# Kernel optimization log

Hardware: AMD Instinct MI355X
Metric: run time of the kernel (lower is better)

Reference implementation:

```python
import jax, jax.numpy as jnp
import numpy as np

D_MODEL = 1024
N_HEADS = 16
HEAD_DIM = D_MODEL // N_HEADS


def setup_inputs() -> dict:
    key = jax.random.key(0)
    ks = jax.random.split(key, 5)
    s = 1.0 / np.sqrt(D_MODEL)
    return {
        "x": jax.random.normal(ks[0], (2, 2048, D_MODEL), dtype=jnp.float32),
        "w_qkv": jax.random.uniform(ks[1], (3 * D_MODEL, D_MODEL), jnp.float32, -s, s),
        "b_qkv": jax.random.uniform(ks[2], (3 * D_MODEL,), jnp.float32, -s, s),
        "w_out": jax.random.uniform(ks[3], (D_MODEL, D_MODEL), jnp.float32, -s, s),
        "b_out": jax.random.uniform(ks[4], (D_MODEL,), jnp.float32, -s, s),
    }


def _attn(x, w_qkv, b_qkv, w_out, b_out):
    bsz, seq_len, _ = x.shape
    qkv = jnp.einsum('bsd,ed->bse', x, w_qkv) + b_qkv  # [B,S,3D]
    q, k, v = jnp.split(qkv, 3, axis=-1)
    def heads(t):  # [B,S,D] -> [B,H,S,Dh]
        return t.reshape(bsz, seq_len, N_HEADS, HEAD_DIM).transpose(0, 2, 1, 3)
    q, k, v = heads(q), heads(k), heads(v)
    scores = jnp.einsum('bhqd,bhkd->bhqk', q, k) / np.sqrt(HEAD_DIM)
    mask = jnp.tril(jnp.ones((seq_len, seq_len), dtype=bool))
    scores = jnp.where(mask, scores, -jnp.inf)
    probs = jax.nn.softmax(scores, axis=-1)
    attn = jnp.einsum('bhqk,bhkd->bhqd', probs, v)
    attn = attn.transpose(0, 2, 1, 3).reshape(bsz, seq_len, D_MODEL)
    return jnp.einsum('bsd,ed->bse', attn, w_out) + b_out


def reference(x, w_qkv, b_qkv, w_out, b_out):
    return _attn(x, w_qkv, b_qkv, w_out, b_out)
```

## Files before the change

kernel.cpp:

```cpp
#include <hip/hip_runtime.h>
#include <hip/hip_bf16.h>
#include <stdint.h>

#define SEQ     2048
#define BATCH   2
#define NHEADS  16
#define HDIM    64
#define DMODEL  1024
#define N3      3072
#define D2      2048
#define MTOT    (BATCH*SEQ)

typedef __attribute__((ext_vector_type(4))) float f32x4;
typedef __attribute__((ext_vector_type(8))) short bf16x8;

static __device__ inline unsigned short f2bf(float f) {
    union { float f; unsigned u; } v; v.f = f;
    unsigned r = (v.u + 0x7fffu + ((v.u >> 16) & 1u)) >> 16;
    return (unsigned short)r;
}
static __device__ inline unsigned pk2bf(float a, float b) {
    union { __hip_bfloat162 h; unsigned u; } c;
    c.h = __float22bfloat162_rn(make_float2(a, b));
    return c.u;
}

#define GLDS(gp, lp) __builtin_amdgcn_global_load_lds( \
    (const __attribute__((address_space(1))) void*)(gp), \
    (__attribute__((address_space(3))) void*)(lp), 16, 0, 0)

__global__ void cast_all(const float* __restrict__ x,
                         const float* __restrict__ wqkv,
                         const float* __restrict__ wout,
                         unsigned short* __restrict__ xb,
                         unsigned short* __restrict__ wqkvb,
                         unsigned short* __restrict__ woutb) {
    long i4 = (long)(blockIdx.x * blockDim.x + threadIdx.x) * 4;
    const float* src; unsigned short* dst; long off;
    if (i4 < 4194304L)      { src = x;    dst = xb;    off = i4; }
    else if (i4 < 7340032L) { src = wqkv; dst = wqkvb; off = i4 - 4194304L; }
    else                    { src = wout; dst = woutb; off = i4 - 7340032L; }
    float4 v = *(const float4*)(src + off);
    union { uint2 u; ushort4 s; } pk;
    pk.u.x = pk2bf(v.x, v.y); pk.u.y = pk2bf(v.z, v.w);
    *(ushort4*)(dst + off) = pk.s;
}

__global__ __launch_bounds__(256, 2) void gemm_qkv(
    const unsigned short* __restrict__ A,
    const unsigned short* __restrict__ B,
    const float* __restrict__ bias,
    unsigned short* __restrict__ qk,
    unsigned short* __restrict__ vT)
{
    __shared__ __align__(16) unsigned short sA[2][128][64];
    __shared__ __align__(16) unsigned short sB[2][128][64];
    const int tid  = threadIdx.x;
    const int wave = tid >> 6, lane = tid & 63;
    const int quad = lane >> 4, l16 = lane & 15, l7 = l16 & 7;
    const int wm = wave >> 1, wn = wave & 1;
    const int m0 = blockIdx.x * 128, n0 = blockIdx.y * 128;

    f32x4 acc[4][4];
    const f32x4 zero = {0.f, 0.f, 0.f, 0.f};
    #pragma unroll
    for (int i = 0; i < 4; i++)
        #pragma unroll
        for (int j = 0; j < 4; j++) acc[i][j] = zero;

    const int rsel = tid >> 3;
    const int sgl  = (tid & 7) ^ (rsel & 7);
    const unsigned short* gA0 = A + (long)(m0 + rsel) * 1024 + sgl * 8;
    const unsigned short* gB0 = B + (long)(n0 + rsel) * 1024 + sgl * 8;

    #pragma unroll
    for (int i = 0; i < 4; i++) {
        GLDS(gA0 + (long)(32 * i) * 1024, &sA[0][32 * i + wave * 8][0]);
        GLDS(gB0 + (long)(32 * i) * 1024, &sB[0][32 * i + wave * 8][0]);
    }

    int buf = 0;
    for (int k0 = 0; k0 < 1024; k0 += 64, buf ^= 1) {
        __syncthreads();
        if (k0 + 64 < 1024) {
            #pragma unroll
            for (int i = 0; i < 4; i++) {
                GLDS(gA0 + (long)(32 * i) * 1024 + k0 + 64, &sA[buf ^ 1][32 * i + wave * 8][0]);
                GLDS(gB0 + (long)(32 * i) * 1024 + k0 + 64, &sB[buf ^ 1][32 * i + wave * 8][0]);
            }
        }
        #pragma unroll
        for (int ks = 0; ks < 2; ks++) {
            bf16x8 af[4], bfr[4];
            #pragma unroll
            for (int mt = 0; mt < 4; mt++)
                af[mt] = *(const bf16x8*)(&sA[buf][wm * 64 + mt * 16 + l16][((ks * 4 + quad) ^ l7) * 8]);
            #pragma unroll
            for (int nt = 0; nt < 4; nt++)
                bfr[nt] = *(const bf16x8*)(&sB[buf][wn * 64 + nt * 16 + l16][((ks * 4 + quad) ^ l7) * 8]);
            #pragma unroll
            for (int mt = 0; mt < 4; mt++)
                #pragma unroll
                for (int nt = 0; nt < 4; nt++)
                    acc[mt][nt] = __builtin_amdgcn_mfma_f32_16x16x32_bf16(
                        af[mt], bfr[nt], acc[mt][nt], 0, 0, 0);
        }
    }

    if (n0 < 2048) {
        #pragma unroll
        for (int nt = 0; nt < 4; nt++) {
            const int n_g = n0 + wn * 64 + nt * 16 + l16;
            const float bv = bias[n_g];
            #pragma unroll
            for (int mt = 0; mt < 4; mt++) {
                #pragma unroll
                for (int r = 0; r < 4; r++) {
                    const int m_g = m0 + wm * 64 + mt * 16 + quad * 4 + r;
                    qk[(long)m_g * D2 + n_g] = f2bf(acc[mt][nt][r] + bv);
                }
            }
        }
    } else {
        const int b = m0 >> 11;
        #pragma unroll
        for (int nt = 0; nt < 4; nt++) {
            const int n_g = n0 + wn * 64 + nt * 16 + l16;
            const int dm = n_g - 2048;
            const long vrow = (long)(((b << 4) + (dm >> 6)) << 6) + (dm & 63);
            const float bv = bias[n_g];
            #pragma unroll
            for (int mt = 0; mt < 4; mt++) {
                const int m_g = m0 + wm * 64 + mt * 16 + quad * 4;
                union { uint2 u; ushort4 s; } pk;
                pk.u.x = pk2bf(acc[mt][nt][0] + bv, acc[mt][nt][1] + bv);
                pk.u.y = pk2bf(acc[mt][nt][2] + bv, acc[mt][nt][3] + bv);
                *(ushort4*)(vT + vrow * D2 + (m_g & 2047)) = pk.s;
            }
        }
    }
}

__global__ __launch_bounds__(256, 2) void gemm_out(
    const unsigned short* __restrict__ A,
    const unsigned short* __restrict__ B,
    const float* __restrict__ bias,
    float* __restrict__ C)
{
    __shared__ __align__(16) unsigned short sA[2][128][64];
    __shared__ __align__(16) unsigned short sB[2][64][64];
    const int tid  = threadIdx.x;
    const int wave = tid >> 6, lane = tid & 63;
    const int quad = lane >> 4, l16 = lane & 15, l7 = l16 & 7;
    const int wm = wave >> 1, wn = wave & 1;
    const int m0 = blockIdx.x * 128, n0 = blockIdx.y * 64;

    f32x4 acc[4][2];
    const f32x4 zero = {0.f, 0.f, 0.f, 0.f};
    #pragma unroll
    for (int i = 0; i < 4; i++) { acc[i][0] = zero; acc[i][1] = zero; }

    const int rsel = tid >> 3;
    const int sgl  = (tid & 7) ^ (rsel & 7);
    const unsigned short* gA0 = A + (long)(m0 + rsel) * 1024 + sgl * 8;
    const unsigned short* gB0 = B + (long)(n0 + rsel) * 1024 + sgl * 8;

    #pragma unroll
    for (int i = 0; i < 4; i++)
        GLDS(gA0 + (long)(32 * i) * 1024, &sA[0][32 * i + wave * 8][0]);
    #pragma unroll
    for (int i = 0; i < 2; i++)
        GLDS(gB0 + (long)(32 * i) * 1024, &sB[0][32 * i + wave * 8][0]);

    int buf = 0;
    for (int k0 = 0; k0 < 1024; k0 += 64, buf ^= 1) {
        __syncthreads();
        if (k0 + 64 < 1024) {
            #pragma unroll
            for (int i = 0; i < 4; i++)
                GLDS(gA0 + (long)(32 * i) * 1024 + k0 + 64, &sA[buf ^ 1][32 * i + wave * 8][0]);
            #pragma unroll
            for (int i = 0; i < 2; i++)
                GLDS(gB0 + (long)(32 * i) * 1024 + k0 + 64, &sB[buf ^ 1][32 * i + wave * 8][0]);
        }
        #pragma unroll
        for (int ks = 0; ks < 2; ks++) {
            bf16x8 af[4], bfr[2];
            #pragma unroll
            for (int mt = 0; mt < 4; mt++)
                af[mt] = *(const bf16x8*)(&sA[buf][wm * 64 + mt * 16 + l16][((ks * 4 + quad) ^ l7) * 8]);
            #pragma unroll
            for (int nt = 0; nt < 2; nt++)
                bfr[nt] = *(const bf16x8*)(&sB[buf][wn * 32 + nt * 16 + l16][((ks * 4 + quad) ^ l7) * 8]);
            #pragma unroll
            for (int mt = 0; mt < 4; mt++)
                #pragma unroll
                for (int nt = 0; nt < 2; nt++)
                    acc[mt][nt] = __builtin_amdgcn_mfma_f32_16x16x32_bf16(
                        af[mt], bfr[nt], acc[mt][nt], 0, 0, 0);
        }
    }
    #pragma unroll
    for (int nt = 0; nt < 2; nt++) {
        const int n_g = n0 + wn * 32 + nt * 16 + l16;
        const float bv = bias[n_g];
        #pragma unroll
        for (int mt = 0; mt < 4; mt++) {
            #pragma unroll
            for (int r = 0; r < 4; r++) {
                const int m_g = m0 + wm * 64 + mt * 16 + quad * 4 + r;
                C[(long)m_g * DMODEL + n_g] = acc[mt][nt][r] + bv;
            }
        }
    }
}

__global__ __launch_bounds__(256, 2) void attn_kernel(
    const unsigned short* __restrict__ qk,
    const unsigned short* __restrict__ vT,
    unsigned short* __restrict__ attn)
{
    __shared__ __align__(16) unsigned short sK [2][2][64][64];
    __shared__ __align__(16) unsigned short sVt[2][2][64][64];
    __shared__ __align__(16) unsigned short sP [4][16][64];

    const int tid  = threadIdx.x;
    const int w    = tid >> 6, lane = tid & 63;
    const int quad = lane >> 4, l16 = lane & 15, l7 = l16 & 7;

    const int bh = blockIdx.x;
    const int b  = bh >> 4, h = bh & 15;
    const int pair = blockIdx.y;
    const long rowb = (long)b * SEQ;

    const int rl = lane >> 3;
    const int sm = (lane & 7) ^ rl;
    const unsigned short* kg = qk + (rowb + w * 16 + rl) * D2 + 1024 + h * HDIM + sm * 8;
    const unsigned short* vg = vT + (long)(bh * 64 + w * 16 + rl) * D2 + sm * 8;

    const int s0 = quad ^ l7;
    const float C2 = 0.18033688011112042f;
    const f32x4 zero = {0.f, 0.f, 0.f, 0.f};

    #pragma unroll
    for (int ph = 0; ph < 2; ph++) {
        const int qtile  = ph ? (31 - pair) : pair;
        const int qbase  = qtile * 64;
        const int ntiles = qtile + 1;
        const int npairs = (ntiles + 1) >> 1;

        bf16x8 qf0, qf1;
        {
            const unsigned short* qp = qk + (rowb + qbase + w * 16 + l16) * D2 + h * HDIM;
            qf0 = *(const bf16x8*)(qp + quad * 8);
            qf1 = *(const bf16x8*)(qp + 32 + quad * 8);
        }
        f32x4 Oacc[4];
        #pragma unroll
        for (int mf = 0; mf < 4; mf++) Oacc[mf] = zero;
        float l_i = 0.f;

        __syncthreads();
        {
            const long o0 = 0, o1 = (long)(1 <= qtile ? 1 : qtile) * 64;
            GLDS(kg + o0 * D2,           &sK [0][0][w * 16][0]);
            GLDS(kg + o0 * D2 + 8L * D2, &sK [0][0][w * 16 + 8][0]);
            GLDS(vg + o0,                &sVt[0][0][w * 16][0]);
            GLDS(vg + o0 + 8L * D2,      &sVt[0][0][w * 16 + 8][0]);
            GLDS(kg + o1 * D2,           &sK [0][1][w * 16][0]);
            GLDS(kg + o1 * D2 + 8L * D2, &sK [0][1][w * 16 + 8][0]);
            GLDS(vg + o1,                &sVt[0][1][w * 16][0]);
            GLDS(vg + o1 + 8L * D2,      &sVt[0][1][w * 16 + 8][0]);
        }

        int buf = 0;
        for (int p = 0; p < npairs; p++, buf ^= 1) {
            __syncthreads();
            if (p + 1 < npairs) {
                const int t0 = 2 * p + 2, t1 = 2 * p + 3;
                const long o0 = (long)(t0 <= qtile ? t0 : qtile) * 64;
                const long o1 = (long)(t1 <= qtile ? t1 : qtile) * 64;
                GLDS(kg + o0 * D2,           &sK [buf ^ 1][0][w * 16][0]);
                GLDS(kg + o0 * D2 + 8L * D2, &sK [buf ^ 1][0][w * 16 + 8][0]);
                GLDS(vg + o0,                &sVt[buf ^ 1][0][w * 16][0]);
                GLDS(vg + o0 + 8L * D2,      &sVt[buf ^ 1][0][w * 16 + 8][0]);
                GLDS(kg + o1 * D2,           &sK [buf ^ 1][1][w * 16][0]);
                GLDS(kg + o1 * D2 + 8L * D2, &sK [buf ^ 1][1][w * 16 + 8][0]);
                GLDS(vg + o1,                &sVt[buf ^ 1][1][w * 16][0]);
                GLDS(vg + o1 + 8L * D2,      &sVt[buf ^ 1][1][w * 16 + 8][0]);
            }
            #pragma unroll
            for (int s = 0; s < 2; s++) {
                const int t = 2 * p + s;
                if (t >= ntiles) break;

                f32x4 st[4];
                #pragma unroll
                for (int kvf = 0; kvf < 4; kvf++) {
                    bf16x8 kf0 = *(const bf16x8*)(&sK[buf][s][kvf * 16 + l16][s0 * 8]);
                    bf16x8 kf1 = *(const bf16x8*)(&sK[buf][s][kvf * 16 + l16][(s0 ^ 4) * 8]);
                    st[kvf] = __builtin_amdgcn_mfma_f32_16x16x32_bf16(kf0, qf0, zero, 0, 0, 0);
                    st[kvf] = __builtin_amdgcn_mfma_f32_16x16x32_bf16(kf1, qf1, st[kvf], 0, 0, 0);
                }
                if (t == qtile) {
                    const int ql = w * 16 + l16;
                    #pragma unroll
                    for (int kvf = 0; kvf < 4; kvf++) {
                        const int kv = kvf * 16 + quad * 4;
                        #pragma unroll
                        for (int r = 0; r < 4; r++)
                            if (kv + r > ql) st[kvf][r] = -1e30f;
                    }
                }
                #pragma unroll
                for (int kvf = 0; kvf < 4; kvf++) {
                    #pragma unroll
                    for (int r = 0; r < 4; r++)
                        st[kvf][r] = __builtin_amdgcn_exp2f(st[kvf][r] * C2);
                }
                f32x4 ps = (st[0] + st[1]) + (st[2] + st[3]);
                l_i += (ps[0] + ps[1]) + (ps[2] + ps[3]);

                #pragma unroll
                for (int kvf = 0; kvf < 4; kvf++) {
                    union { uint2 u; ushort4 s4; } pk;
                    pk.u.x = pk2bf(st[kvf][0], st[kvf][1]);
                    pk.u.y = pk2bf(st[kvf][2], st[kvf][3]);
                    const int seg = (kvf * 2 + (quad >> 1)) ^ l7;
                    *(ushort4*)(&sP[w][l16][seg * 8 + (quad & 1) * 4]) = pk.s4;
                }
                bf16x8 pf0 = *(const bf16x8*)(&sP[w][l16][(quad ^ l7) * 8]);
                bf16x8 pf1 = *(const bf16x8*)(&sP[w][l16][((4 + quad) ^ l7) * 8]);
                #pragma unroll
                for (int mf = 0; mf < 4; mf++) {
                    bf16x8 vf0 = *(const bf16x8*)(&sVt[buf][s][mf * 16 + l16][s0 * 8]);
                    bf16x8 vf1 = *(const bf16x8*)(&sVt[buf][s][mf * 16 + l16][(s0 ^ 4) * 8]);
                    Oacc[mf] = __builtin_amdgcn_mfma_f32_16x16x32_bf16(vf0, pf0, Oacc[mf], 0, 0, 0);
                    Oacc[mf] = __builtin_amdgcn_mfma_f32_16x16x32_bf16(vf1, pf1, Oacc[mf], 0, 0, 0);
                }
            }
        }
        float L = l_i;
        L += __shfl_xor(L, 16);
        L += __shfl_xor(L, 32);
        const float inv = 1.0f / L;
        const int q = qbase + w * 16 + l16;
        unsigned short* op = attn + (rowb + q) * DMODEL + h * HDIM + quad * 4;
        #pragma unroll
        for (int mf = 0; mf < 4; mf++) {
            union { uint2 u; ushort4 s4; } pk;
            pk.u.x = pk2bf(Oacc[mf][0] * inv, Oacc[mf][1] * inv);
            pk.u.y = pk2bf(Oacc[mf][2] * inv, Oacc[mf][3] * inv);
            *(ushort4*)(op + mf * 16) = pk.s4;
        }
    }
}

extern "C" void kernel_launch(void* const* d_in, const int* in_sizes, int n_in,
                              void* d_out, int out_size, void* d_ws, size_t ws_size,
                              hipStream_t stream) {
    const float* x    = (const float*)d_in[0];
    const float* wqkv = (const float*)d_in[1];
    const float* bqkv = (const float*)d_in[2];
    const float* wout = (const float*)d_in[3];
    const float* bout = (const float*)d_in[4];

    char* ws = (char*)d_ws;
    unsigned short* xb    = (unsigned short*)(ws);
    unsigned short* wqkvb = (unsigned short*)(ws + (8L << 20));
    unsigned short* woutb = (unsigned short*)(ws + (14L << 20));
    unsigned short* qkb   = (unsigned short*)(ws + (16L << 20));
    unsigned short* vTb   = (unsigned short*)(ws + (32L << 20));
    unsigned short* attnb = (unsigned short*)(ws + (40L << 20));

    cast_all<<<8192, 256, 0, stream>>>(x, wqkv, wout, xb, wqkvb, woutb);

    dim3 g1(32, 24);
    gemm_qkv<<<g1, 256, 0, stream>>>(xb, wqkvb, bqkv, qkb, vTb);

    dim3 g2(32, 16);
    attn_kernel<<<g2, 256, 0, stream>>>(qkb, vTb, attnb);

    dim3 g3(32, 16);
    gemm_out<<<g3, 256, 0, stream>>>(attnb, woutb, bout, (float*)d_out);
}
```

Before: 175.6 us.

## Enlarge QKV GEMM tiles to 256x256 with 8 waves and explicit waitcnt pipelining

The QKV projection GEMM now uses 256x256 output tiles per 512-thread block, with each wave owning a 128x64 sub-tile. Blocks are numbered M-fastest over a 1D grid. The main loop issues the next K-tile's global-to-LDS loads before computing the current one, using manual vmcnt/lgkmcnt waits and raw s_barriers instead of __syncthreads. The aim is more operand reuse per LDS load and fewer, larger blocks (192 instead of 768), at the cost of one block per CU and higher register pressure from 32 accumulators per lane.

```diff
diff --git a/kernel.cpp b/kernel.cpp
--- a/kernel.cpp
+++ b/kernel.cpp
@@ -46,66 +46,98 @@
     *(ushort4*)(dst + off) = pk.s;
 }
 
-__global__ __launch_bounds__(256, 2) void gemm_qkv(
+__global__ __launch_bounds__(512, 1) void gemm_qkv(
     const unsigned short* __restrict__ A,
     const unsigned short* __restrict__ B,
     const float* __restrict__ bias,
     unsigned short* __restrict__ qk,
     unsigned short* __restrict__ vT)
 {
-    __shared__ __align__(16) unsigned short sA[2][128][64];
-    __shared__ __align__(16) unsigned short sB[2][128][64];
+    __shared__ __align__(16) unsigned short sA[2][256][64];
+    __shared__ __align__(16) unsigned short sB[2][256][64];
     const int tid  = threadIdx.x;
-    const int wave = tid >> 6, lane = tid & 63;
+    const int w    = tid >> 6, lane = tid & 63;
     const int quad = lane >> 4, l16 = lane & 15, l7 = l16 & 7;
-    const int wm = wave >> 1, wn = wave & 1;
-    const int m0 = blockIdx.x * 128, n0 = blockIdx.y * 128;
-
-    f32x4 acc[4][4];
+    const int wm = w >> 2, wn = w & 3;
+    const int bid = blockIdx.x;
+    const int m0 = (bid & 15) << 8;
+    const int n0 = (bid >> 4) << 8;
+
+    f32x4 acc[8][4];
     const f32x4 zero = {0.f, 0.f, 0.f, 0.f};
     #pragma unroll
-    for (int i = 0; i < 4; i++)
+    for (int i = 0; i < 8; i++)
         #pragma unroll
         for (int j = 0; j < 4; j++) acc[i][j] = zero;
 
     const int rsel = tid >> 3;
     const int sgl  = (tid & 7) ^ (rsel & 7);
-    const unsigned short* gA0 = A + (long)(m0 + rsel) * 1024 + sgl * 8;
-    const unsigned short* gB0 = B + (long)(n0 + rsel) * 1024 + sgl * 8;
-
-    #pragma unroll
-    for (int i = 0; i < 4; i++) {
-        GLDS(gA0 + (long)(32 * i) * 1024, &sA[0][32 * i + wave * 8][0]);
-        GLDS(gB0 + (long)(32 * i) * 1024, &sB[0][32 * i + wave * 8][0]);
-    }
-
-    int buf = 0;
-    for (int k0 = 0; k0 < 1024; k0 += 64, buf ^= 1) {
-        __syncthreads();
-        if (k0 + 64 < 1024) {
-            #pragma unroll
-            for (int i = 0; i < 4; i++) {
-                GLDS(gA0 + (long)(32 * i) * 1024 + k0 + 64, &sA[buf ^ 1][32 * i + wave * 8][0]);
-                GLDS(gB0 + (long)(32 * i) * 1024 + k0 + 64, &sB[buf ^ 1][32 * i + wave * 8][0]);
-            }
-        }
-        #pragma unroll
-        for (int ks = 0; ks < 2; ks++) {
-            bf16x8 af[4], bfr[4];
-            #pragma unroll
-            for (int mt = 0; mt < 4; mt++)
-                af[mt] = *(const bf16x8*)(&sA[buf][wm * 64 + mt * 16 + l16][((ks * 4 + quad) ^ l7) * 8]);
-            #pragma unroll
-            for (int nt = 0; nt < 4; nt++)
-                bfr[nt] = *(const bf16x8*)(&sB[buf][wn * 64 + nt * 16 + l16][((ks * 4 + quad) ^ l7) * 8]);
-            #pragma unroll
-            for (int mt = 0; mt < 4; mt++)
-                #pragma unroll
-                for (int nt = 0; nt < 4; nt++)
-                    acc[mt][nt] = __builtin_amdgcn_mfma_f32_16x16x32_bf16(
-                        af[mt], bfr[nt], acc[mt][nt], 0, 0, 0);
-        }
-    }
+    const unsigned short* gA = A + (long)(m0 + rsel) * 1024 + sgl * 8;
+    const unsigned short* gB = B + (long)(n0 + rsel) * 1024 + sgl * 8;
+
+    #pragma unroll
+    for (int j = 0; j < 4; j++) {
+        GLDS(gA + (long)(64 * j) * 1024, &sA[0][64 * j + w * 8][0]);
+        GLDS(gB + (long)(64 * j) * 1024, &sB[0][64 * j + w * 8][0]);
+    }
+
+    auto compute_tile = [&](const unsigned short (*A_)[64],
+                            const unsigned short (*B_)[64]) {
+        #pragma unroll
+        for (int mh = 0; mh < 2; mh++) {
+            bf16x8 af[4][2];
+            #pragma unroll
+            for (int mt2 = 0; mt2 < 4; mt2++)
+                #pragma unroll
+                for (int kk = 0; kk < 2; kk++)
+                    af[mt2][kk] = *(const bf16x8*)(
+                        &A_[wm * 128 + mh * 64 + mt2 * 16 + l16]
+                           [(((kk << 2) + quad) ^ l7) * 8]);
+            #pragma unroll
+            for (int nh = 0; nh < 2; nh++) {
+                bf16x8 bfr[2][2];
+                #pragma unroll
+                for (int nt2 = 0; nt2 < 2; nt2++)
+                    #pragma unroll
+                    for (int kk = 0; kk < 2; kk++)
+                        bfr[nt2][kk] = *(const bf16x8*)(
+                            &B_[wn * 64 + nh * 32 + nt2 * 16 + l16]
+                               [(((kk << 2) + quad) ^ l7) * 8]);
+                #pragma unroll
+                for (int mt2 = 0; mt2 < 4; mt2++)
+                    #pragma unroll
+                    for (int nt2 = 0; nt2 < 2; nt2++)
+                        #pragma unroll
+                        for (int kk = 0; kk < 2; kk++)
+                            acc[mh * 4 + mt2][nh * 2 + nt2] =
+                                __builtin_amdgcn_mfma_f32_16x16x32_bf16(
+                                    af[mt2][kk], bfr[nt2][kk],
+                                    acc[mh * 4 + mt2][nh * 2 + nt2], 0, 0, 0);
+            }
+        }
+    };
+
+    for (int t = 0; t < 15; ++t) {
+        const int nb = (t + 1) & 1, cb = t & 1;
+        const long ko = (long)(t + 1) * 64;
+        #pragma unroll
+        for (int j = 0; j < 4; j++) {
+            GLDS(gA + (long)(64 * j) * 1024 + ko, &sA[nb][64 * j + w * 8][0]);
+            GLDS(gB + (long)(64 * j) * 1024 + ko, &sB[nb][64 * j + w * 8][0]);
+        }
+        __builtin_amdgcn_sched_barrier(0);
+        asm volatile("s_waitcnt vmcnt(8)" ::: "memory");
+        __builtin_amdgcn_sched_barrier(0);
+        __builtin_amdgcn_s_barrier();
+        compute_tile(sA[cb], sB[cb]);
+        asm volatile("s_waitcnt lgkmcnt(0)" ::: "memory");
+        __builtin_amdgcn_sched_barrier(0);
+        __builtin_amdgcn_s_barrier();
+    }
+    asm volatile("s_waitcnt vmcnt(0)" ::: "memory");
+    __builtin_amdgcn_sched_barrier(0);
+    __builtin_amdgcn_s_barrier();
+    compute_tile(sA[1], sB[1]);
 
     if (n0 < 2048) {
         #pragma unroll
@@ -113,10 +145,10 @@
             const int n_g = n0 + wn * 64 + nt * 16 + l16;
             const float bv = bias[n_g];
             #pragma unroll
-            for (int mt = 0; mt < 4; mt++) {
+            for (int mt = 0; mt < 8; mt++) {
                 #pragma unroll
                 for (int r = 0; r < 4; r++) {
-                    const int m_g = m0 + wm * 64 + mt * 16 + quad * 4 + r;
+                    const int m_g = m0 + wm * 128 + mt * 16 + quad * 4 + r;
                     qk[(long)m_g * D2 + n_g] = f2bf(acc[mt][nt][r] + bv);
                 }
             }
@@ -130,8 +162,8 @@
             const long vrow = (long)(((b << 4) + (dm >> 6)) << 6) + (dm & 63);
             const float bv = bias[n_g];
             #pragma unroll
-            for (int mt = 0; mt < 4; mt++) {
-                const int m_g = m0 + wm * 64 + mt * 16 + quad * 4;
+            for (int mt = 0; mt < 8; mt++) {
+                const int m_g = m0 + wm * 128 + mt * 16 + quad * 4;
                 union { uint2 u; ushort4 s; } pk;
                 pk.u.x = pk2bf(acc[mt][nt][0] + bv, acc[mt][nt][1] + bv);
                 pk.u.y = pk2bf(acc[mt][nt][2] + bv, acc[mt][nt][3] + bv);
@@ -375,8 +407,7 @@
 
     cast_all<<<8192, 256, 0, stream>>>(x, wqkv, wout, xb, wqkvb, woutb);
 
-    dim3 g1(32, 24);
-    gemm_qkv<<<g1, 256, 0, stream>>>(xb, wqkvb, bqkv, qkb, vTb);
+    gemm_qkv<<<192, 512, 0, stream>>>(xb, wqkvb, bqkv, qkb, vTb);
 
     dim3 g2(32, 16);
     attn_kernel<<<g2, 256, 0, stream>>>(qkb, vTb, attnb);
```

Measured after the change: 175.8 us. About the same (+0.1%).
